# Kernel tuning notes

Hardware: AMD Instinct MI355X
Metric: run time of the kernel (lower is better)

The kernel has to match this reference:

```python
import jax, jax.numpy as jnp
import numpy as np

K = 3          # neighbors for interpolation (torch_geometric default)
BIG = 1e10     # masks cross-batch pairs out of the kNN search
EPS = 1e-16    # clamp on squared distance before inverting (PyG knn_interpolate)


def setup_inputs() -> dict:
    key = jax.random.key(0)
    ks = jax.random.split(key, 8)
    N, M, C_IN, C_SKIP, H = 4096, 16384, 256, 128, 256
    x = jax.random.normal(ks[0], (N, C_IN), dtype=jnp.float32)
    pos = jax.random.normal(ks[1], (N, 3), dtype=jnp.float32)
    batch = jnp.zeros((N,), dtype=jnp.int64)
    x_skip = jax.random.normal(ks[2], (M, C_SKIP), dtype=jnp.float32)
    pos_skip = jax.random.normal(ks[3], (M, 3), dtype=jnp.float32)
    batch_skip = jnp.zeros((M,), dtype=jnp.int64)
    # MLP params: Linear(384->256) + ReLU + Linear(256->256)
    W1 = jax.random.normal(ks[4], (C_IN + C_SKIP, H), dtype=jnp.float32) * (1.0 / np.sqrt(C_IN + C_SKIP))
    b1 = jnp.zeros((H,), dtype=jnp.float32)
    W2 = jax.random.normal(ks[5], (H, H), dtype=jnp.float32) * (1.0 / np.sqrt(H))
    b2 = jnp.zeros((H,), dtype=jnp.float32)
    return {"x": x, "pos": pos, "batch": batch, "x_skip": x_skip,
            "pos_skip": pos_skip, "batch_skip": batch_skip,
            "W1": W1, "b1": b1, "W2": W2, "b2": b2}


def knn_interpolate(x, pos, pos_skip, batch, batch_skip, k):
    # squared pairwise distances [M, N] via ||q||^2 + ||p||^2 - 2 q.p (avoids [M,N,3])
    qq = jnp.sum(pos_skip * pos_skip, axis=1, keepdims=True)      # [M,1]
    pp = jnp.sum(pos * pos, axis=1)                               # [N]
    d2 = qq + pp[None, :] - 2.0 * (pos_skip @ pos.T)              # [M,N]
    d2 = d2 + jnp.where(batch_skip[:, None] != batch[None, :], BIG, 0.0)
    _, idx = jax.lax.top_k(-d2, k)                                # [M,k] nearest indices
    # recompute exact squared distances for the chosen neighbors
    nbr_pos = pos[idx]                                            # [M,k,3]
    d2k = jnp.sum((pos_skip[:, None, :] - nbr_pos) ** 2, axis=-1) # [M,k]
    w = 1.0 / jnp.clip(d2k, EPS)                                  # inverse-distance weights
    nbr_x = x[idx]                                                # [M,k,C]
    y = jnp.einsum('mk,mkc->mc', w, nbr_x) / jnp.sum(w, axis=1, keepdims=True)
    return y


def reference(x, pos, batch, x_skip, pos_skip, batch_skip, W1, b1, W2, b2):
    y = knn_interpolate(x, pos, pos_skip, batch, batch_skip, K)   # [M, C_in]
    h = jnp.concatenate([y, x_skip], axis=1)                      # [M, C_in+C_skip]
    h = jax.nn.relu(h @ W1 + b1)
    out = h @ W2 + b2
    return (out, pos_skip, batch_skip)
```

## Files before the change

kernel.cpp:

```cpp
#include <hip/hip_runtime.h>
#include <hip/hip_bf16.h>

#define N_PTS  4096
#define M_Q    16384
#define C_IN   256
#define C_SKIP 128
#define C_H    384
#define HDIM   256
#define NSPLIT 32
#define PTS_PER_SPLIT (N_PTS / NSPLIT)

typedef __bf16 bf16x8 __attribute__((ext_vector_type(8)));
typedef __bf16 bf16x4 __attribute__((ext_vector_type(4)));
typedef float  f32x4  __attribute__((ext_vector_type(4)));

__device__ __forceinline__ __bf16 tobf(float f) {
    __hip_bfloat16 h = __float2bfloat16(f);
    __bf16 r;
    __builtin_memcpy(&r, &h, 2);
    return r;
}

__device__ __forceinline__ void insert3(float d, int j,
                                        float& b0, float& b1, float& b2,
                                        int& i0, int& i1, int& i2) {
    if (d < b2) {
        if (d < b1) {
            b2 = b1; i2 = i1;
            if (d < b0) { b1 = b0; i1 = i0; b0 = d; i0 = j; }
            else        { b1 = d;  i1 = j; }
        } else { b2 = d; i2 = j; }
    }
}

__global__ __launch_bounds__(256) void prep_kernel(
        const float* __restrict__ W1, const float* __restrict__ W2,
        const float* __restrict__ pos,
        __bf16* __restrict__ W1t, __bf16* __restrict__ W2t,
        float4* __restrict__ pos4) {
    const int i = blockIdx.x * 256 + threadIdx.x;
    if (i < C_H * HDIM) {
        const int k = i / HDIM, n = i % HDIM;
        W1t[n * C_H + k] = tobf(W1[i]);
    } else if (i < C_H * HDIM + HDIM * HDIM) {
        const int j = i - C_H * HDIM;
        const int k = j / HDIM, n = j % HDIM;
        W2t[n * HDIM + k] = tobf(W2[j]);
    } else if (i < C_H * HDIM + HDIM * HDIM + N_PTS) {
        const int j = i - (C_H * HDIM + HDIM * HDIM);
        const float px = pos[j*3+0], py = pos[j*3+1], pz = pos[j*3+2];
        pos4[j] = make_float4(px, py, pz, px*px + py*py + pz*pz);
    }
}

__global__ __launch_bounds__(256) void knn_part_kernel(
        const float4* __restrict__ pos4, const float* __restrict__ pos_skip,
        float* __restrict__ cand_d, int* __restrict__ cand_i) {
    const int s  = blockIdx.y;
    const int qa = blockIdx.x * 512 + threadIdx.x;
    const int qb = qa + 256;
    const int j0 = s * PTS_PER_SPLIT;
    const float ax = -2.0f * pos_skip[qa*3+0];
    const float ay = -2.0f * pos_skip[qa*3+1];
    const float az = -2.0f * pos_skip[qa*3+2];
    const float bx = -2.0f * pos_skip[qb*3+0];
    const float by = -2.0f * pos_skip[qb*3+1];
    const float bz = -2.0f * pos_skip[qb*3+2];
    float A0 = 3e38f, A1 = 3e38f, A2 = 3e38f;
    float B0 = 3e38f, B1 = 3e38f, B2 = 3e38f;
    int   ia0 = 0, ia1 = 0, ia2 = 0, ib0 = 0, ib1 = 0, ib2 = 0;
    #pragma unroll 8
    for (int j = 0; j < PTS_PER_SPLIT; ++j) {
        const float4 p = pos4[j0 + j];
        const float dA = fmaf(p.x, ax, fmaf(p.y, ay, fmaf(p.z, az, p.w)));
        const float dB = fmaf(p.x, bx, fmaf(p.y, by, fmaf(p.z, bz, p.w)));
        const int  jj = j0 + j;
        {
            const bool c2 = dA < A2, c1 = dA < A1, c0 = dA < A0;
            A2 = c2 ? (c1 ? A1 : dA) : A2;  ia2 = c2 ? (c1 ? ia1 : jj) : ia2;
            A1 = c1 ? (c0 ? A0 : dA) : A1;  ia1 = c1 ? (c0 ? ia0 : jj) : ia1;
            A0 = c0 ? dA : A0;              ia0 = c0 ? jj : ia0;
        }
        {
            const bool c2 = dB < B2, c1 = dB < B1, c0 = dB < B0;
            B2 = c2 ? (c1 ? B1 : dB) : B2;  ib2 = c2 ? (c1 ? ib1 : jj) : ib2;
            B1 = c1 ? (c0 ? B0 : dB) : B1;  ib1 = c1 ? (c0 ? ib0 : jj) : ib1;
            B0 = c0 ? dB : B0;              ib0 = c0 ? jj : ib0;
        }
    }
    const int SM = NSPLIT * M_Q;
    const int basea = s * M_Q + qa;
    const int baseb = s * M_Q + qb;
    cand_d[0*SM + basea] = A0;  cand_d[0*SM + baseb] = B0;
    cand_d[1*SM + basea] = A1;  cand_d[1*SM + baseb] = B1;
    cand_d[2*SM + basea] = A2;  cand_d[2*SM + baseb] = B2;
    cand_i[0*SM + basea] = ia0; cand_i[0*SM + baseb] = ib0;
    cand_i[1*SM + basea] = ia1; cand_i[1*SM + baseb] = ib1;
    cand_i[2*SM + basea] = ia2; cand_i[2*SM + baseb] = ib2;
}

__global__ __launch_bounds__(256) void merge_interp_kernel(
        const float* __restrict__ cand_d, const int* __restrict__ cand_i,
        const float* __restrict__ pos, const float* __restrict__ pos_skip,
        const float* __restrict__ x, const float* __restrict__ x_skip,
        __bf16* __restrict__ h, float* __restrict__ out, int out_size) {
    __shared__ int   sIdx[64][3];
    __shared__ float sW[64][3];
    const int t  = threadIdx.x;
    const int ql = t >> 2, l = t & 3;
    const int m0 = blockIdx.x * 64;
    const int q  = m0 + ql;

    float b0 = 3e38f, b1 = 3e38f, b2 = 3e38f;
    int   i0 = 0, i1 = 0, i2 = 0;
    const int SM = NSPLIT * M_Q;
    #pragma unroll
    for (int u = 0; u < NSPLIT/4; ++u) {
        const int s = l * (NSPLIT/4) + u;
        const int base = s * M_Q + q;
        const float d0 = cand_d[0*SM + base], d1 = cand_d[1*SM + base], d2c = cand_d[2*SM + base];
        const int   j0 = cand_i[0*SM + base], j1 = cand_i[1*SM + base], j2c = cand_i[2*SM + base];
        insert3(d0, j0,  b0,b1,b2, i0,i1,i2);
        insert3(d1, j1,  b0,b1,b2, i0,i1,i2);
        insert3(d2c, j2c, b0,b1,b2, i0,i1,i2);
    }
    #pragma unroll
    for (int m = 1; m <= 2; m <<= 1) {
        const float nb0 = __shfl_xor(b0, m), nb1 = __shfl_xor(b1, m), nb2 = __shfl_xor(b2, m);
        const int   ni0 = __shfl_xor(i0, m), ni1 = __shfl_xor(i1, m), ni2 = __shfl_xor(i2, m);
        const bool upper = (l & m) != 0;
        float e0 = upper ? b0 : nb0, e1 = upper ? b1 : nb1, e2 = upper ? b2 : nb2;
        int   f0 = upper ? i0 : ni0, f1 = upper ? i1 : ni1, f2 = upper ? i2 : ni2;
        if (upper) { b0 = nb0; b1 = nb1; b2 = nb2; i0 = ni0; i1 = ni1; i2 = ni2; }
        insert3(e0, f0, b0,b1,b2, i0,i1,i2);
        insert3(e1, f1, b0,b1,b2, i0,i1,i2);
        insert3(e2, f2, b0,b1,b2, i0,i1,i2);
    }
    if (l == 0) {
        const float qx = pos_skip[q*3+0], qy = pos_skip[q*3+1], qz = pos_skip[q*3+2];
        float w[3]; int ii[3] = {i0, i1, i2};
        float wsum = 0.0f;
        #pragma unroll
        for (int r = 0; r < 3; ++r) {
            const float dx = qx - pos[ii[r]*3+0];
            const float dy = qy - pos[ii[r]*3+1];
            const float dz = qz - pos[ii[r]*3+2];
            const float d2 = dx*dx + dy*dy + dz*dz;
            w[r] = 1.0f / fmaxf(d2, 1e-16f);
            wsum += w[r];
        }
        const float inv = 1.0f / wsum;
        #pragma unroll
        for (int r = 0; r < 3; ++r) { sIdx[ql][r] = ii[r]; sW[ql][r] = w[r] * inv; }
    }
    __syncthreads();

    #pragma unroll 4
    for (int g = 0; g < 24; ++g) {
        const int flat = g * 256 + t;
        const int r  = flat / 96;
        const int c4 = flat % 96;
        const int m  = m0 + r;
        if (c4 < 64) {
            const int c = c4 * 4;
            const int   j0 = sIdx[r][0], j1 = sIdx[r][1], j2 = sIdx[r][2];
            const float w0 = sW[r][0],   w1 = sW[r][1],   w2 = sW[r][2];
            const float4 v0 = *(const float4*)(x + (size_t)j0 * C_IN + c);
            const float4 v1 = *(const float4*)(x + (size_t)j1 * C_IN + c);
            const float4 v2 = *(const float4*)(x + (size_t)j2 * C_IN + c);
            bf16x4 o;
            o[0] = tobf(w0*v0.x + w1*v1.x + w2*v2.x);
            o[1] = tobf(w0*v0.y + w1*v1.y + w2*v2.y);
            o[2] = tobf(w0*v0.z + w1*v1.z + w2*v2.z);
            o[3] = tobf(w0*v0.w + w1*v1.w + w2*v2.w);
            *(bf16x4*)(h + (size_t)m * C_H + c) = o;
        } else {
            const int c = (c4 - 64) * 4;
            const float4 v = *(const float4*)(x_skip + (size_t)m * C_SKIP + c);
            bf16x4 o;
            o[0] = tobf(v.x); o[1] = tobf(v.y); o[2] = tobf(v.z); o[3] = tobf(v.w);
            *(bf16x4*)(h + (size_t)m * C_H + C_IN + c) = o;
        }
    }

    if (t < 64 * 3)
        out[(size_t)M_Q * HDIM + m0*3 + t] = pos_skip[m0*3 + t];
    const int zbase = M_Q * HDIM + M_Q * 3;
    const int ztot  = out_size - zbase;
    const int chunk = (ztot + 255) / 256;
    for (int i2z = t; i2z < chunk; i2z += 256) {
        const int gi = blockIdx.x * chunk + i2z;
        if (gi < ztot) out[zbase + gi] = 0.0f;
    }
}

template<bool RELU, int KDIM, typename OUT_T>
__global__ __launch_bounds__(256) void gemm_bf16_kernel(
        const __bf16* __restrict__ A, const __bf16* __restrict__ Bt,
        const float* __restrict__ bias, OUT_T* __restrict__ C) {
    __shared__ __bf16 As[2][64][40];
    __shared__ __bf16 Bs[2][128][40];
    const int t    = threadIdx.x;
    const int w    = t >> 6;
    const int lane = t & 63;
    const int ln = lane & 15, kq = lane >> 4;
    const int m0 = blockIdx.y * 64;
    const int n0 = blockIdx.x * 128;
    const int wm = (w >> 1) * 32;
    const int wn = (w & 1) * 64;

    const int rA = t >> 1, cA = (t & 1) * 16;
    constexpr int KS = KDIM / 32;
    int4 a0{}, a1{}, b0v, b1v;
    if (t < 128) {
        a0 = *(const int4*)(A + (size_t)(m0 + rA) * KDIM + cA);
        a1 = *(const int4*)(A + (size_t)(m0 + rA) * KDIM + cA + 8);
    }
    b0v = *(const int4*)(Bt + (size_t)(n0 + rA) * KDIM + cA);
    b1v = *(const int4*)(Bt + (size_t)(n0 + rA) * KDIM + cA + 8);

    f32x4 acc[2][4] = {};

    for (int ks = 0; ks < KS; ++ks) {
        const int p = ks & 1;
        if (t < 128) {
            *(int4*)&As[p][rA][cA]     = a0;
            *(int4*)&As[p][rA][cA + 8] = a1;
        }
        *(int4*)&Bs[p][rA][cA]     = b0v;
        *(int4*)&Bs[p][rA][cA + 8] = b1v;
        __syncthreads();
        if (ks + 1 < KS) {
            const int k0 = (ks + 1) * 32;
            if (t < 128) {
                a0 = *(const int4*)(A + (size_t)(m0 + rA) * KDIM + k0 + cA);
                a1 = *(const int4*)(A + (size_t)(m0 + rA) * KDIM + k0 + cA + 8);
            }
            b0v = *(const int4*)(Bt + (size_t)(n0 + rA) * KDIM + k0 + cA);
            b1v = *(const int4*)(Bt + (size_t)(n0 + rA) * KDIM + k0 + cA + 8);
        }
        bf16x8 af[2], bfv[4];
        #pragma unroll
        for (int mt = 0; mt < 2; ++mt)
            af[mt] = *(const bf16x8*)&As[p][wm + mt*16 + ln][kq*8];
        #pragma unroll
        for (int nt = 0; nt < 4; ++nt)
            bfv[nt] = *(const bf16x8*)&Bs[p][wn + nt*16 + ln][kq*8];
        #pragma unroll
        for (int mt = 0; mt < 2; ++mt)
            #pragma unroll
            for (int nt = 0; nt < 4; ++nt)
                acc[mt][nt] = __builtin_amdgcn_mfma_f32_16x16x32_bf16(
                                  af[mt], bfv[nt], acc[mt][nt], 0, 0, 0);
    }

    #pragma unroll
    for (int nt = 0; nt < 4; ++nt) {
        const int n = n0 + wn + nt*16 + ln;
        const float bv = bias[n];
        #pragma unroll
        for (int mt = 0; mt < 2; ++mt) {
            const int mbase = m0 + wm + mt*16 + kq*4;
            #pragma unroll
            for (int r = 0; r < 4; ++r) {
                float v = acc[mt][nt][r] + bv;
                if (RELU) v = fmaxf(v, 0.0f);
                C[(size_t)(mbase + r) * 256 + n] = (OUT_T)v;
            }
        }
    }
}

extern "C" void kernel_launch(void* const* d_in, const int* in_sizes, int n_in,
                              void* d_out, int out_size, void* d_ws, size_t ws_size,
                              hipStream_t stream) {
    (void)in_sizes; (void)n_in; (void)ws_size;
    const float* x        = (const float*)d_in[0];
    const float* pos      = (const float*)d_in[1];
    const float* x_skip   = (const float*)d_in[3];
    const float* pos_skip = (const float*)d_in[4];
    const float* W1       = (const float*)d_in[6];
    const float* b1       = (const float*)d_in[7];
    const float* W2       = (const float*)d_in[8];
    const float* b2       = (const float*)d_in[9];
    float* out = (float*)d_out;

    char* ws = (char*)d_ws;
    float*  cand_d = (float*) (ws);
    int*    cand_i = (int*)   (ws + 6291456);
    __bf16* h      = (__bf16*)(ws + 12582912);
    __bf16* hid    = (__bf16*)(ws + 25165824);
    __bf16* W1t    = (__bf16*)(ws + 33554432);
    __bf16* W2t    = (__bf16*)(ws + 33751040);
    float4* pos4   = (float4*)(ws + 33882112);

    prep_kernel     <<<(C_H*HDIM + HDIM*HDIM + N_PTS + 255)/256, 256, 0, stream>>>(
        W1, W2, pos, W1t, W2t, pos4);
    knn_part_kernel <<<dim3(M_Q/512, NSPLIT), 256, 0, stream>>>(pos4, pos_skip, cand_d, cand_i);
    merge_interp_kernel<<<M_Q/64, 256, 0, stream>>>(
        cand_d, cand_i, pos, pos_skip, x, x_skip, h, out, out_size);
    gemm_bf16_kernel<true, C_H, __bf16><<<dim3(2, M_Q/64), 256, 0, stream>>>(
        h, W1t, b1, (__bf16*)hid);
    gemm_bf16_kernel<false, HDIM, float><<<dim3(2, M_Q/64), 256, 0, stream>>>(
        hid, W2t, b2, out);
}
```

Before: 165.9 us.

## Fuse all stages into one cooperative persistent kernel with grid syncs

Turns the five separate launches (prep, kNN partial search, merge/interpolate, two GEMMs) into one cooperative kernel of 512 blocks that steps through the stages with grid-wide syncs. The goal is to remove per-launch overhead and the gaps between kernels. In exchange, stages that used many blocks (such as the 1024-block kNN) now loop over fewer persistent blocks, half the blocks sit idle during the merge stage, and each grid.sync costs something. Occupancy and shared memory are also capped by the combined kernel. If cooperative launch is unavailable, the code falls back to the original multi-kernel path.

```diff
diff --git a/kernel.cpp b/kernel.cpp
--- a/kernel.cpp
+++ b/kernel.cpp
@@ -1,5 +1,8 @@
 #include <hip/hip_runtime.h>
+#include <hip/hip_cooperative_groups.h>
 #include <hip/hip_bf16.h>
+
+namespace cg = cooperative_groups;
 
 #define N_PTS  4096
 #define M_Q    16384
@@ -9,6 +12,7 @@
 #define HDIM   256
 #define NSPLIT 32
 #define PTS_PER_SPLIT (N_PTS / NSPLIT)
+#define GRID   512
 
 typedef __bf16 bf16x8 __attribute__((ext_vector_type(8)));
 typedef __bf16 bf16x4 __attribute__((ext_vector_type(4)));
@@ -33,12 +37,12 @@
     }
 }
 
-__global__ __launch_bounds__(256) void prep_kernel(
+
+__device__ __forceinline__ void prep_body(int i,
         const float* __restrict__ W1, const float* __restrict__ W2,
         const float* __restrict__ pos,
         __bf16* __restrict__ W1t, __bf16* __restrict__ W2t,
         float4* __restrict__ pos4) {
-    const int i = blockIdx.x * 256 + threadIdx.x;
     if (i < C_H * HDIM) {
         const int k = i / HDIM, n = i % HDIM;
         W1t[n * C_H + k] = tobf(W1[i]);
@@ -53,19 +57,18 @@
     }
 }
 
-__global__ __launch_bounds__(256) void knn_part_kernel(
+__device__ __forceinline__ void knn_body(int s, int xb, int t,
         const float4* __restrict__ pos4, const float* __restrict__ pos_skip,
         float* __restrict__ cand_d, int* __restrict__ cand_i) {
-    const int s  = blockIdx.y;
-    const int qa = blockIdx.x * 512 + threadIdx.x;
-    const int qb = qa + 256;
+    const int qa = xb * 512 + t;
+    const int qb2 = qa + 256;
     const int j0 = s * PTS_PER_SPLIT;
     const float ax = -2.0f * pos_skip[qa*3+0];
     const float ay = -2.0f * pos_skip[qa*3+1];
     const float az = -2.0f * pos_skip[qa*3+2];
-    const float bx = -2.0f * pos_skip[qb*3+0];
-    const float by = -2.0f * pos_skip[qb*3+1];
-    const float bz = -2.0f * pos_skip[qb*3+2];
+    const float bx = -2.0f * pos_skip[qb2*3+0];
+    const float by = -2.0f * pos_skip[qb2*3+1];
+    const float bz = -2.0f * pos_skip[qb2*3+2];
     float A0 = 3e38f, A1 = 3e38f, A2 = 3e38f;
     float B0 = 3e38f, B1 = 3e38f, B2 = 3e38f;
     int   ia0 = 0, ia1 = 0, ia2 = 0, ib0 = 0, ib1 = 0, ib2 = 0;
@@ -90,7 +93,7 @@
     }
     const int SM = NSPLIT * M_Q;
     const int basea = s * M_Q + qa;
-    const int baseb = s * M_Q + qb;
+    const int baseb = s * M_Q + qb2;
     cand_d[0*SM + basea] = A0;  cand_d[0*SM + baseb] = B0;
     cand_d[1*SM + basea] = A1;  cand_d[1*SM + baseb] = B1;
     cand_d[2*SM + basea] = A2;  cand_d[2*SM + baseb] = B2;
@@ -99,18 +102,15 @@
     cand_i[2*SM + basea] = ia2; cand_i[2*SM + baseb] = ib2;
 }
 
-__global__ __launch_bounds__(256) void merge_interp_kernel(
+__device__ __forceinline__ void merge_interp_body(int m0, int t,
+        int* sIdx, float* sW,
         const float* __restrict__ cand_d, const int* __restrict__ cand_i,
         const float* __restrict__ pos, const float* __restrict__ pos_skip,
         const float* __restrict__ x, const float* __restrict__ x_skip,
-        __bf16* __restrict__ h, float* __restrict__ out, int out_size) {
-    __shared__ int   sIdx[64][3];
-    __shared__ float sW[64][3];
-    const int t  = threadIdx.x;
+        __bf16* __restrict__ h, float* __restrict__ out, int out_size,
+        int nblocks, int bid) {
     const int ql = t >> 2, l = t & 3;
-    const int m0 = blockIdx.x * 64;
     const int q  = m0 + ql;
-
     float b0 = 3e38f, b1 = 3e38f, b2 = 3e38f;
     int   i0 = 0, i1 = 0, i2 = 0;
     const int SM = NSPLIT * M_Q;
@@ -138,7 +138,7 @@
     }
     if (l == 0) {
         const float qx = pos_skip[q*3+0], qy = pos_skip[q*3+1], qz = pos_skip[q*3+2];
-        float w[3]; int ii[3] = {i0, i1, i2};
+        float wv[3]; int ii[3] = {i0, i1, i2};
         float wsum = 0.0f;
         #pragma unroll
         for (int r = 0; r < 3; ++r) {
@@ -146,12 +146,12 @@
             const float dy = qy - pos[ii[r]*3+1];
             const float dz = qz - pos[ii[r]*3+2];
             const float d2 = dx*dx + dy*dy + dz*dz;
-            w[r] = 1.0f / fmaxf(d2, 1e-16f);
-            wsum += w[r];
+            wv[r] = 1.0f / fmaxf(d2, 1e-16f);
+            wsum += wv[r];
         }
         const float inv = 1.0f / wsum;
         #pragma unroll
-        for (int r = 0; r < 3; ++r) { sIdx[ql][r] = ii[r]; sW[ql][r] = w[r] * inv; }
+        for (int r = 0; r < 3; ++r) { sIdx[ql*3+r] = ii[r]; sW[ql*3+r] = wv[r] * inv; }
     }
     __syncthreads();
 
@@ -163,8 +163,8 @@
         const int m  = m0 + r;
         if (c4 < 64) {
             const int c = c4 * 4;
-            const int   j0 = sIdx[r][0], j1 = sIdx[r][1], j2 = sIdx[r][2];
-            const float w0 = sW[r][0],   w1 = sW[r][1],   w2 = sW[r][2];
+            const int   j0 = sIdx[r*3+0], j1 = sIdx[r*3+1], j2 = sIdx[r*3+2];
+            const float w0 = sW[r*3+0],   w1 = sW[r*3+1],   w2 = sW[r*3+2];
             const float4 v0 = *(const float4*)(x + (size_t)j0 * C_IN + c);
             const float4 v1 = *(const float4*)(x + (size_t)j1 * C_IN + c);
             const float4 v2 = *(const float4*)(x + (size_t)j2 * C_IN + c);
@@ -187,29 +187,27 @@
         out[(size_t)M_Q * HDIM + m0*3 + t] = pos_skip[m0*3 + t];
     const int zbase = M_Q * HDIM + M_Q * 3;
     const int ztot  = out_size - zbase;
-    const int chunk = (ztot + 255) / 256;
-    for (int i2z = t; i2z < chunk; i2z += 256) {
-        const int gi = blockIdx.x * chunk + i2z;
+    const int chunk = (ztot + nblocks - 1) / nblocks;
+    for (int iz = t; iz < chunk; iz += 256) {
+        const int gi = bid * chunk + iz;
         if (gi < ztot) out[zbase + gi] = 0.0f;
     }
 }
 
 template<bool RELU, int KDIM, typename OUT_T>
-__global__ __launch_bounds__(256) void gemm_bf16_kernel(
+__device__ __forceinline__ void gemm_body(int m0, int n0, int t,
+        __bf16* smem,
         const __bf16* __restrict__ A, const __bf16* __restrict__ Bt,
         const float* __restrict__ bias, OUT_T* __restrict__ C) {
-    __shared__ __bf16 As[2][64][40];
-    __shared__ __bf16 Bs[2][128][40];
-    const int t    = threadIdx.x;
+    __bf16* As = smem;
+    __bf16* Bs = smem + 5120;
     const int w    = t >> 6;
     const int lane = t & 63;
     const int ln = lane & 15, kq = lane >> 4;
-    const int m0 = blockIdx.y * 64;
-    const int n0 = blockIdx.x * 128;
     const int wm = (w >> 1) * 32;
     const int wn = (w & 1) * 64;
-
     const int rA = t >> 1, cA = (t & 1) * 16;
+
     constexpr int KS = KDIM / 32;
     int4 a0{}, a1{}, b0v, b1v;
     if (t < 128) {
@@ -224,11 +222,11 @@
     for (int ks = 0; ks < KS; ++ks) {
         const int p = ks & 1;
         if (t < 128) {
-            *(int4*)&As[p][rA][cA]     = a0;
-            *(int4*)&As[p][rA][cA + 8] = a1;
-        }
-        *(int4*)&Bs[p][rA][cA]     = b0v;
-        *(int4*)&Bs[p][rA][cA + 8] = b1v;
+            *(int4*)&As[p*2560 + rA*40 + cA]     = a0;
+            *(int4*)&As[p*2560 + rA*40 + cA + 8] = a1;
+        }
+        *(int4*)&Bs[p*5120 + rA*40 + cA]     = b0v;
+        *(int4*)&Bs[p*5120 + rA*40 + cA + 8] = b1v;
         __syncthreads();
         if (ks + 1 < KS) {
             const int k0 = (ks + 1) * 32;
@@ -242,10 +240,10 @@
         bf16x8 af[2], bfv[4];
         #pragma unroll
         for (int mt = 0; mt < 2; ++mt)
-            af[mt] = *(const bf16x8*)&As[p][wm + mt*16 + ln][kq*8];
+            af[mt] = *(const bf16x8*)&As[p*2560 + (wm + mt*16 + ln)*40 + kq*8];
         #pragma unroll
         for (int nt = 0; nt < 4; ++nt)
-            bfv[nt] = *(const bf16x8*)&Bs[p][wn + nt*16 + ln][kq*8];
+            bfv[nt] = *(const bf16x8*)&Bs[p*5120 + (wn + nt*16 + ln)*40 + kq*8];
         #pragma unroll
         for (int mt = 0; mt < 2; ++mt)
             #pragma unroll
@@ -269,6 +267,78 @@
             }
         }
     }
+}
+
+__global__ __launch_bounds__(256, 4) void mega_kernel(
+        const float* __restrict__ x, const float* __restrict__ pos,
+        const float* __restrict__ x_skip, const float* __restrict__ pos_skip,
+        const float* __restrict__ W1, const float* __restrict__ b1,
+        const float* __restrict__ W2, const float* __restrict__ b2,
+        float* __restrict__ out, int out_size,
+        float* __restrict__ cand_d, int* __restrict__ cand_i,
+        __bf16* __restrict__ h, __bf16* __restrict__ hid,
+        __bf16* __restrict__ W1t, __bf16* __restrict__ W2t,
+        float4* __restrict__ pos4) {
+    __shared__ __align__(16) char smem[30720];
+    cg::grid_group grid = cg::this_grid();
+    const int b = blockIdx.x;
+    const int t = threadIdx.x;
+
+    for (int i = b * 256 + t; i < C_H*HDIM + HDIM*HDIM + N_PTS; i += GRID * 256)
+        prep_body(i, W1, W2, pos, W1t, W2t, pos4);
+    grid.sync();
+
+    for (int u = b; u < NSPLIT * 32; u += GRID)
+        knn_body(u >> 5, u & 31, t, pos4, pos_skip, cand_d, cand_i);
+    grid.sync();
+
+    if (b < 256)
+        merge_interp_body(b * 64, t, (int*)smem, (float*)(smem + 768),
+                          cand_d, cand_i, pos, pos_skip, x, x_skip,
+                          h, out, out_size, 256, b);
+    grid.sync();
+
+    gemm_body<true, C_H, __bf16>((b >> 1) * 64, (b & 1) * 128, t,
+                                 (__bf16*)smem, h, W1t, b1, hid);
+    grid.sync();
+
+    gemm_body<false, HDIM, float>((b >> 1) * 64, (b & 1) * 128, t,
+                                  (__bf16*)smem, hid, W2t, b2, out);
+}
+
+__global__ __launch_bounds__(256) void prep_kernel(
+        const float* __restrict__ W1, const float* __restrict__ W2,
+        const float* __restrict__ pos,
+        __bf16* __restrict__ W1t, __bf16* __restrict__ W2t,
+        float4* __restrict__ pos4) {
+    prep_body(blockIdx.x * 256 + threadIdx.x, W1, W2, pos, W1t, W2t, pos4);
+}
+
+__global__ __launch_bounds__(256) void knn_part_kernel(
+        const float4* __restrict__ pos4, const float* __restrict__ pos_skip,
+        float* __restrict__ cand_d, int* __restrict__ cand_i) {
+    knn_body(blockIdx.y, blockIdx.x, threadIdx.x, pos4, pos_skip, cand_d, cand_i);
+}
+
+__global__ __launch_bounds__(256) void merge_interp_kernel(
+        const float* __restrict__ cand_d, const int* __restrict__ cand_i,
+        const float* __restrict__ pos, const float* __restrict__ pos_skip,
+        const float* __restrict__ x, const float* __restrict__ x_skip,
+        __bf16* __restrict__ h, float* __restrict__ out, int out_size) {
+    __shared__ int   sIdx[64 * 3];
+    __shared__ float sW[64 * 3];
+    merge_interp_body(blockIdx.x * 64, threadIdx.x, sIdx, sW,
+                      cand_d, cand_i, pos, pos_skip, x, x_skip,
+                      h, out, out_size, 256, blockIdx.x);
+}
+
+template<bool RELU, int KDIM, typename OUT_T>
+__global__ __launch_bounds__(256) void gemm_bf16_kernel(
+        const __bf16* __restrict__ A, const __bf16* __restrict__ Bt,
+        const float* __restrict__ bias, OUT_T* __restrict__ C) {
+    __shared__ __align__(16) __bf16 smem[15360];
+    gemm_body<RELU, KDIM, OUT_T>(blockIdx.y * 64, blockIdx.x * 128, threadIdx.x,
+                                 smem, A, Bt, bias, C);
 }
 
 extern "C" void kernel_launch(void* const* d_in, const int* in_sizes, int n_in,
@@ -294,13 +364,35 @@
     __bf16* W2t    = (__bf16*)(ws + 33751040);
     float4* pos4   = (float4*)(ws + 33882112);
 
-    prep_kernel     <<<(C_H*HDIM + HDIM*HDIM + N_PTS + 255)/256, 256, 0, stream>>>(
-        W1, W2, pos, W1t, W2t, pos4);
-    knn_part_kernel <<<dim3(M_Q/512, NSPLIT), 256, 0, stream>>>(pos4, pos_skip, cand_d, cand_i);
-    merge_interp_kernel<<<M_Q/64, 256, 0, stream>>>(
-        cand_d, cand_i, pos, pos_skip, x, x_skip, h, out, out_size);
-    gemm_bf16_kernel<true, C_H, __bf16><<<dim3(2, M_Q/64), 256, 0, stream>>>(
-        h, W1t, b1, (__bf16*)hid);
-    gemm_bf16_kernel<false, HDIM, float><<<dim3(2, M_Q/64), 256, 0, stream>>>(
-        hid, W2t, b2, out);
-}
+    bool coop = false;
+    int numCU = 0, maxBlk = 0;
+    if (hipDeviceGetAttribute(&numCU, hipDeviceAttributeMultiprocessorCount, 0) == hipSuccess &&
+        hipOccupancyMaxActiveBlocksPerMultiprocessor(&maxBlk, (const void*)mega_kernel, 256, 0) == hipSuccess) {
+        coop = ((long)numCU * maxBlk >= GRID);
+    }
+
+    if (coop) {
+        void* args[] = {
+            (void*)&x, (void*)&pos, (void*)&x_skip, (void*)&pos_skip,
+            (void*)&W1, (void*)&b1, (void*)&W2, (void*)&b2,
+            (void*)&out, (void*)&out_size,
+            (void*)&cand_d, (void*)&cand_i, (void*)&h, (void*)&hid,
+            (void*)&W1t, (void*)&W2t, (void*)&pos4
+        };
+        if (hipLaunchCooperativeKernel((const void*)mega_kernel,
+                                       dim3(GRID), dim3(256), args, 0, stream) != hipSuccess)
+            coop = false;
+    }
+
+    if (!coop) {
+        prep_kernel     <<<(C_H*HDIM + HDIM*HDIM + N_PTS + 255)/256, 256, 0, stream>>>(
+            W1, W2, pos, W1t, W2t, pos4);
+        knn_part_kernel <<<dim3(M_Q/512, NSPLIT), 256, 0, stream>>>(pos4, pos_skip, cand_d, cand_i);
+        merge_interp_kernel<<<M_Q/64, 256, 0, stream>>>(
+            cand_d, cand_i, pos, pos_skip, x, x_skip, h, out, out_size);
+        gemm_bf16_kernel<true, C_H, __bf16><<<dim3(2, M_Q/64), 256, 0, stream>>>(
+            h, W1t, b1, hid);
+        gemm_bf16_kernel<false, HDIM, float><<<dim3(2, M_Q/64), 256, 0, stream>>>(
+            hid, W2t, b2, out);
+    }
+}
```

Result: slower. 402.1 us (+142.3%).
